# Optimization experiments

Hardware: AMD Instinct MI355X
Metric: run time of the kernel (lower is better)

The kernel has to match this reference:

```python
import jax, jax.numpy as jnp
import numpy as np
from jax import lax

INPUT_DIM = 16
H1 = 5
H2 = 50
NUM_CLASSES = 20
B = 4096
T = 512


def _lstm(x, w_ih, w_hh, b_ih, b_hh, hidden):
    # x: [B, T, D]; PyTorch LSTM gate order i, f, g, o; returns all hidden states [B, T, H]
    xg = jnp.einsum('btd,gd->btg', x, w_ih) + (b_ih + b_hh)  # [B, T, 4H]
    xg_t = jnp.swapaxes(xg, 0, 1)  # [T, B, 4H]
    h0 = jnp.zeros((x.shape[0], hidden), x.dtype)
    c0 = jnp.zeros((x.shape[0], hidden), x.dtype)

    def step(carry, xt):
        h, c = carry
        g = xt + h @ w_hh.T  # [B, 4H]
        i, f, gg, o = jnp.split(g, 4, axis=-1)
        i = jax.nn.sigmoid(i)
        f = jax.nn.sigmoid(f)
        gg = jnp.tanh(gg)
        o = jax.nn.sigmoid(o)
        c = f * c + i * gg
        h = o * jnp.tanh(c)
        return (h, c), h

    _, hs = lax.scan(step, (h0, c0), xg_t)
    return jnp.swapaxes(hs, 0, 1)  # [B, T, H]


def setup_inputs() -> dict:
    key = jax.random.key(0)
    ks = jax.random.split(key, 12)
    s1 = 1.0 / np.sqrt(H1)
    s2 = 1.0 / np.sqrt(H2)
    u = lambda k, shape, s: jax.random.uniform(k, shape, jnp.float32, -s, s)
    return {
        'x': jax.random.normal(ks[0], (B, T, INPUT_DIM), jnp.float32),
        'w_ih1': u(ks[1], (4 * H1, INPUT_DIM), s1),
        'w_hh1': u(ks[2], (4 * H1, H1), s1),
        'b_ih1': u(ks[3], (4 * H1,), s1),
        'b_hh1': u(ks[4], (4 * H1,), s1),
        'w_ih2': u(ks[5], (4 * H2, H1), s2),
        'w_hh2': u(ks[6], (4 * H2, H2), s2),
        'b_ih2': u(ks[7], (4 * H2,), s2),
        'b_hh2': u(ks[8], (4 * H2,), s2),
        'fc_w': u(ks[9], (NUM_CLASSES, H2), s2),
        'fc_b': u(ks[10], (NUM_CLASSES,), s2),
    }


def reference(x, w_ih1, w_hh1, b_ih1, b_hh1, w_ih2, w_hh2, b_ih2, b_hh2, fc_w, fc_b):
    h1 = _lstm(x, w_ih1, w_hh1, b_ih1, b_hh1, H1)   # [B, T, 5]
    h2 = _lstm(h1, w_ih2, w_hh2, b_ih2, b_hh2, H2)  # [B, T, 50]
    feat = h2[:, -1, :]  # last timestep; dropout is identity in eval mode
    out = feat @ fc_w.T + fc_b  # [B, num_classes]
    return (out, feat)
```

## Files before the change

### kernel.cpp

```cpp
#include <hip/hip_runtime.h>
#include <stdint.h>

#define B_TOTAL 4096
#define T_STEPS 512
#define IN_DIM 16
#define H1 5
#define H2 50
#define NCLS 20

typedef __attribute__((ext_vector_type(8))) short bf16x8;
typedef __attribute__((ext_vector_type(4))) float f32x4;

#define LOG2E 1.44269504f
#define C2L   2.88539008f

__device__ inline float rcp1pexp2(float y){
  return __builtin_amdgcn_rcpf(1.0f + __builtin_amdgcn_exp2f(y));
}

__device__ inline unsigned pack_top(float a, float b){
  return __builtin_amdgcn_perm(__float_as_uint(a), __float_as_uint(b), 0x07060302u);
}
__device__ inline void cvt_store(unsigned short* dh, unsigned short* dl, float4 v){
  uint2 H, L;
  H.x = pack_top(v.y, v.x);
  H.y = pack_top(v.w, v.z);
  float r0 = v.x - __uint_as_float(__float_as_uint(v.x) & 0xFFFF0000u);
  float r1 = v.y - __uint_as_float(__float_as_uint(v.y) & 0xFFFF0000u);
  float r2 = v.z - __uint_as_float(__float_as_uint(v.z) & 0xFFFF0000u);
  float r3 = v.w - __uint_as_float(__float_as_uint(v.w) & 0xFFFF0000u);
  L.x = pack_top(r1, r0);
  L.y = pack_top(r3, r2);
  *(uint2*)dh = H; *(uint2*)dl = L;
}
__device__ inline void split1(float h, unsigned short& hi, unsigned short& lo){
  unsigned u = __float_as_uint(h);
  hi = (unsigned short)(u >> 16);
  float r = h - __uint_as_float(u & 0xFFFF0000u);
  lo = (unsigned short)(__float_as_uint(r) >> 16);
}
__device__ inline void wsplit(float w, short& hi, short& lo){
  unsigned u = __float_as_uint(w);
  hi = (short)(u >> 16);
  float r = w - __uint_as_float(u & 0xFFFF0000u);
  lo = (short)(__float_as_uint(r) >> 16);
}

#define LDS_FENCE() __asm__ volatile("s_waitcnt lgkmcnt(0)" ::: "memory")
#define BARRIER()   __asm__ volatile("s_barrier" ::: "memory")

__global__ __launch_bounds__(320, 1) void lstm_fused_kernel(
    const float* __restrict__ x,
    const float* __restrict__ w_ih1, const float* __restrict__ w_hh1,
    const float* __restrict__ b_ih1, const float* __restrict__ b_hh1,
    const float* __restrict__ w_ih2, const float* __restrict__ w_hh2,
    const float* __restrict__ b_ih2, const float* __restrict__ b_hh2,
    const float* __restrict__ fc_w, const float* __restrict__ fc_b,
    float* __restrict__ out)
{
  const int tid  = threadIdx.x;
  const int lane = tid & 63;
  const int wave = tid >> 6;
  const int l15  = lane & 15;
  const int quad = lane >> 4;
  const int b0   = blockIdx.x * 16;

  __shared__ __align__(16) unsigned short a2h[2][16*72], a2l[2][16*72];
  __shared__ __align__(16) unsigned short xrh[8][16*24], xrl[8][16*24];
  __shared__ __align__(16) unsigned short a1h[16*24], a1l[16*24];
  __shared__ float h2f[16*52];

  bf16x8 Bh[4][2], Bl[4][2];
  float bias[4];
  float cst[4] = {0.f,0.f,0.f,0.f};
  const int cg = wave*16 + l15;

  if (wave < 4){
    bool valid = cg < H2;
#pragma unroll
    for (int tt=0; tt<4; ++tt){
      const float gsc = (tt == 2) ? C2L : LOG2E;
      int grow = tt*H2 + cg;
#pragma unroll
      for (int kt=0; kt<2; ++kt){
#pragma unroll
        for (int j=0;j<8;j++){
          int kk = kt*32 + quad*8 + j;
          float w = 0.f;
          if (valid){
            if (kk < H2)         w = w_hh2[grow*H2 + kk];
            else if (kk < H2+H1) w = w_ih2[grow*H1 + (kk-H2)];
          }
          w *= gsc;
          short hi, lo; wsplit(w, hi, lo);
          Bh[tt][kt][j] = hi; Bl[tt][kt][j] = lo;
        }
      }
      bias[tt] = valid ? gsc * (b_ih2[grow] + b_hh2[grow]) : 0.f;
    }
  } else {
    bool valid = l15 < H1;
#pragma unroll
    for (int tt=0; tt<4; ++tt){
      const float gsc = (tt == 2) ? C2L : LOG2E;
      int grow = tt*H1 + l15;
#pragma unroll
      for (int j=0;j<8;j++){
        int kk = quad*8 + j;
        float w = 0.f;
        if (valid){
          if (kk < IN_DIM)         w = w_ih1[grow*IN_DIM + kk];
          else if (kk < IN_DIM+H1) w = w_hh1[grow*H1 + (kk-IN_DIM)];
        }
        w *= gsc;
        short hi, lo; wsplit(w, hi, lo);
        Bh[tt][0][j] = hi; Bl[tt][0][j] = lo;
        Bh[tt][1][j] = 0;  Bl[tt][1][j] = 0;
      }
      bias[tt] = valid ? gsc * (b_ih1[grow] + b_hh1[grow]) : 0.f;
    }
  }

  f32x4 biasv[4];
#pragma unroll
  for (int tt=0; tt<4; ++tt){
    biasv[tt][0] = bias[tt]; biasv[tt][1] = bias[tt];
    biasv[tt][2] = bias[tt]; biasv[tt][3] = bias[tt];
  }
  const f32x4 zero4 = {0.f,0.f,0.f,0.f};

  { unsigned short* p = &a2h[0][0]; for (int i=tid;i<2*16*72;i+=320) p[i]=0; }
  { unsigned short* p = &a2l[0][0]; for (int i=tid;i<2*16*72;i+=320) p[i]=0; }
  { unsigned short* p = &a1h[0];    for (int i=tid;i<16*24;i+=320)   p[i]=0; }
  { unsigned short* p = &a1l[0];    for (int i=tid;i<16*24;i+=320)   p[i]=0; }

  const int xb = lane >> 2;
  const int xd = (lane & 3) * 4;
  if (wave == 4){
#pragma unroll
    for (int s=0;s<8;s++){
      float4 v = *(const float4*)&x[((size_t)(b0+xb)*T_STEPS + s)*IN_DIM + xd];
      cvt_store(&xrh[s][xb*24+xd], &xrl[s][xb*24+xd], v);
    }
  }
  __syncthreads();

  float4 pf0, pf1, pf2, pf3;
  bool pend = false;

#define ACT_BLOCK(ACC_, HV_) \
    _Pragma("unroll") \
    for (int r=0;r<4;r++){ \
      float gi = rcp1pexp2(-ACC_[0][r]); \
      float gf = rcp1pexp2(-ACC_[1][r]); \
      float gg = fmaf(-2.0f, rcp1pexp2(ACC_[2][r]), 1.0f); \
      float go = rcp1pexp2(-ACC_[3][r]); \
      cst[r] = fmaf(gf, cst[r], gi * (C2L * gg)); \
      HV_[r] = go * fmaf(-2.0f, rcp1pexp2(cst[r]), 1.0f); \
    }

#define LSTM2_BODY(T_, RD_, WR_) do { \
    const int rb = l15*72; \
    bf16x8 ah0 = *(const bf16x8*)&a2h[RD_][rb +      quad*8]; \
    bf16x8 al0 = *(const bf16x8*)&a2l[RD_][rb +      quad*8]; \
    bf16x8 ah1 = *(const bf16x8*)&a2h[RD_][rb + 32 + quad*8]; \
    bf16x8 al1 = *(const bf16x8*)&a2l[RD_][rb + 32 + quad*8]; \
    f32x4 acc[4]; \
    _Pragma("unroll") \
    for (int tt=0; tt<4; ++tt){ \
      f32x4 c0 = __builtin_amdgcn_mfma_f32_16x16x32_bf16(ah0, Bh[tt][0], biasv[tt], 0,0,0); \
      c0 = __builtin_amdgcn_mfma_f32_16x16x32_bf16(al0, Bh[tt][0], c0, 0,0,0); \
      c0 = __builtin_amdgcn_mfma_f32_16x16x32_bf16(ah0, Bl[tt][0], c0, 0,0,0); \
      f32x4 c1 = __builtin_amdgcn_mfma_f32_16x16x32_bf16(ah1, Bh[tt][1], zero4, 0,0,0); \
      c1 = __builtin_amdgcn_mfma_f32_16x16x32_bf16(al1, Bh[tt][1], c1, 0,0,0); \
      c1 = __builtin_amdgcn_mfma_f32_16x16x32_bf16(ah1, Bl[tt][1], c1, 0,0,0); \
      acc[tt] = c0 + c1; \
    } \
    float hv[4]; \
    ACT_BLOCK(acc, hv) \
    if (cg < H2){ \
      const int wrb = quad*4*72 + cg; \
      _Pragma("unroll") \
      for (int r=0;r<4;r++){ \
        unsigned short hh, hl; split1(hv[r], hh, hl); \
        a2h[WR_][wrb + r*72] = hh; \
        a2l[WR_][wrb + r*72] = hl; \
      } \
      if ((T_) == T_STEPS-1){ \
        _Pragma("unroll") \
        for (int r=0;r<4;r++){ \
          out[(size_t)B_TOTAL*NCLS + (size_t)(b0+quad*4+r)*H2 + cg] = hv[r]; \
          h2f[(quad*4+r)*52 + cg] = hv[r]; \
        } \
      } \
    } \
  } while(0)

#define LSTM1_BODY(T_, WR_) do { \
    const int s = (T_) + 1; \
    if (s < T_STEPS){ \
      if ((s & 3) == 0 && s+4 < T_STEPS){ \
        const float* xp = &x[((size_t)(b0+xb)*T_STEPS + (s+4))*IN_DIM + xd]; \
        pf0 = *(const float4*)(xp + 0*IN_DIM); \
        pf1 = *(const float4*)(xp + 1*IN_DIM); \
        pf2 = *(const float4*)(xp + 2*IN_DIM); \
        pf3 = *(const float4*)(xp + 3*IN_DIM); \
        pend = true; \
      } \
      const int slot = s & 7; \
      bf16x8 ah, al; \
      if (quad < 2){ \
        ah = *(const bf16x8*)&xrh[slot][l15*24 + quad*8]; \
        al = *(const bf16x8*)&xrl[slot][l15*24 + quad*8]; \
      } else { \
        ah = *(const bf16x8*)&a1h[l15*24 + (quad-2)*8]; \
        al = *(const bf16x8*)&a1l[l15*24 + (quad-2)*8]; \
      } \
      f32x4 acc[4]; \
      _Pragma("unroll") \
      for (int tt=0; tt<4; ++tt){ \
        f32x4 c0 = __builtin_amdgcn_mfma_f32_16x16x32_bf16(ah, Bh[tt][0], biasv[tt], 0,0,0); \
        c0 = __builtin_amdgcn_mfma_f32_16x16x32_bf16(al, Bh[tt][0], c0, 0,0,0); \
        c0 = __builtin_amdgcn_mfma_f32_16x16x32_bf16(ah, Bl[tt][0], c0, 0,0,0); \
        acc[tt] = c0; \
      } \
      float hv[4]; \
      ACT_BLOCK(acc, hv) \
      if (l15 < H1){ \
        _Pragma("unroll") \
        for (int r=0;r<4;r++){ \
          unsigned short hh, hl; split1(hv[r], hh, hl); \
          const int row = quad*4 + r; \
          a1h[row*24 + l15] = hh; \
          a1l[row*24 + l15] = hl; \
          a2h[WR_][row*72 + H2 + l15] = hh; \
          a2l[WR_][row*72 + H2 + l15] = hl; \
        } \
      } \
      if ((s & 3) == 2 && pend){ \
        cvt_store(&xrh[(s+2)&7][xb*24+xd], &xrl[(s+2)&7][xb*24+xd], pf0); \
        cvt_store(&xrh[(s+3)&7][xb*24+xd], &xrl[(s+3)&7][xb*24+xd], pf1); \
        cvt_store(&xrh[(s+4)&7][xb*24+xd], &xrl[(s+4)&7][xb*24+xd], pf2); \
        cvt_store(&xrh[(s+5)&7][xb*24+xd], &xrl[(s+5)&7][xb*24+xd], pf3); \
        pend = false; \
      } \
    } \
  } while(0)

  if (wave == 4) LSTM1_BODY(-1, 0);
  LDS_FENCE(); BARRIER();

  for (int t2 = 0; t2 < T_STEPS; t2 += 2){
    if (wave == 4) LSTM1_BODY(t2, 1);
    else           LSTM2_BODY(t2, 0, 1);
    LDS_FENCE(); BARRIER();
    if (wave == 4) LSTM1_BODY(t2+1, 0);
    else           LSTM2_BODY(t2+1, 1, 0);
    LDS_FENCE(); BARRIER();
  }

#undef LSTM2_BODY
#undef LSTM1_BODY
#undef ACT_BLOCK

  __syncthreads();
  {
    int b = tid / 20, o = tid % 20;
    float s = fc_b[o];
#pragma unroll 10
    for (int k=0;k<H2;k++) s += fc_w[o*H2+k] * h2f[b*52+k];
    out[(size_t)(b0+b)*NCLS + o] = s;
  }
}

extern "C" void kernel_launch(void* const* d_in, const int* in_sizes, int n_in,
                              void* d_out, int out_size, void* d_ws, size_t ws_size,
                              hipStream_t stream) {
  const float* x     = (const float*)d_in[0];
  const float* w_ih1 = (const float*)d_in[1];
  const float* w_hh1 = (const float*)d_in[2];
  const float* b_ih1 = (const float*)d_in[3];
  const float* b_hh1 = (const float*)d_in[4];
  const float* w_ih2 = (const float*)d_in[5];
  const float* w_hh2 = (const float*)d_in[6];
  const float* b_ih2 = (const float*)d_in[7];
  const float* b_hh2 = (const float*)d_in[8];
  const float* fc_w  = (const float*)d_in[9];
  const float* fc_b  = (const float*)d_in[10];
  float* out = (float*)d_out;

  lstm_fused_kernel<<<dim3(B_TOTAL/16), dim3(320), 0, stream>>>(
      x, w_ih1, w_hh1, b_ih1, b_hh1, w_ih2, w_hh2, b_ih2, b_hh2, fc_w, fc_b, out);
}
```

Baseline: 633.8 us.

## Fold layer-1 LSTM into fourth wave alongside last layer-2 columns, drop fifth wave

The block shrinks from five waves to four. Wave 3 now computes the last two layer-2 hidden columns and all five layer-1 units in the same MFMA tile, using a third K-slice for the x input. x is now kept in registers through a rotating two-step prefetch instead of being staged in LDS ring buffers. The tanh gate scale is folded into the fma constants. The intent is to cut the wave count per barrier and remove the LDS staging for x and h1. In exchange, wave 3 does 50% more MFMAs per step and may become the critical path.

Result: faster. 605.1 us (-4.5%).

```diff
diff --git a/kernel.cpp b/kernel.cpp
--- a/kernel.cpp
+++ b/kernel.cpp
@@ -13,26 +13,12 @@
 
 #define LOG2E 1.44269504f
 #define C2L   2.88539008f
+#define C2L2  5.77078016f
 
 __device__ inline float rcp1pexp2(float y){
   return __builtin_amdgcn_rcpf(1.0f + __builtin_amdgcn_exp2f(y));
 }
 
-__device__ inline unsigned pack_top(float a, float b){
-  return __builtin_amdgcn_perm(__float_as_uint(a), __float_as_uint(b), 0x07060302u);
-}
-__device__ inline void cvt_store(unsigned short* dh, unsigned short* dl, float4 v){
-  uint2 H, L;
-  H.x = pack_top(v.y, v.x);
-  H.y = pack_top(v.w, v.z);
-  float r0 = v.x - __uint_as_float(__float_as_uint(v.x) & 0xFFFF0000u);
-  float r1 = v.y - __uint_as_float(__float_as_uint(v.y) & 0xFFFF0000u);
-  float r2 = v.z - __uint_as_float(__float_as_uint(v.z) & 0xFFFF0000u);
-  float r3 = v.w - __uint_as_float(__float_as_uint(v.w) & 0xFFFF0000u);
-  L.x = pack_top(r1, r0);
-  L.y = pack_top(r3, r2);
-  *(uint2*)dh = H; *(uint2*)dl = L;
-}
 __device__ inline void split1(float h, unsigned short& hi, unsigned short& lo){
   unsigned u = __float_as_uint(h);
   hi = (unsigned short)(u >> 16);
@@ -45,11 +31,22 @@
   float r = w - __uint_as_float(u & 0xFFFF0000u);
   lo = (short)(__float_as_uint(r) >> 16);
 }
+__device__ inline void xsplit(float4 a, float4 b, bf16x8& H, bf16x8& L){
+  short h,l;
+  wsplit(a.x,h,l); H[0]=h; L[0]=l;
+  wsplit(a.y,h,l); H[1]=h; L[1]=l;
+  wsplit(a.z,h,l); H[2]=h; L[2]=l;
+  wsplit(a.w,h,l); H[3]=h; L[3]=l;
+  wsplit(b.x,h,l); H[4]=h; L[4]=l;
+  wsplit(b.y,h,l); H[5]=h; L[5]=l;
+  wsplit(b.z,h,l); H[6]=h; L[6]=l;
+  wsplit(b.w,h,l); H[7]=h; L[7]=l;
+}
 
 #define LDS_FENCE() __asm__ volatile("s_waitcnt lgkmcnt(0)" ::: "memory")
 #define BARRIER()   __asm__ volatile("s_barrier" ::: "memory")
 
-__global__ __launch_bounds__(320, 1) void lstm_fused_kernel(
+__global__ __launch_bounds__(256, 1) void lstm_fused_kernel(
     const float* __restrict__ x,
     const float* __restrict__ w_ih1, const float* __restrict__ w_hh1,
     const float* __restrict__ b_ih1, const float* __restrict__ b_hh1,
@@ -66,120 +63,157 @@
   const int b0   = blockIdx.x * 16;
 
   __shared__ __align__(16) unsigned short a2h[2][16*72], a2l[2][16*72];
-  __shared__ __align__(16) unsigned short xrh[8][16*24], xrl[8][16*24];
-  __shared__ __align__(16) unsigned short a1h[16*24], a1l[16*24];
   __shared__ float h2f[16*52];
 
-  bf16x8 Bh[4][2], Bl[4][2];
-  float bias[4];
+  const bf16x8 zero8 = {0,0,0,0,0,0,0,0};
+  const f32x4  zero4 = {0.f,0.f,0.f,0.f};
+
+  bf16x8 Bh[4][3], Bl[4][3];
+  f32x4 biasv[4];
   float cst[4] = {0.f,0.f,0.f,0.f};
-  const int cg = wave*16 + l15;
-
-  if (wave < 4){
-    bool valid = cg < H2;
+
+#pragma unroll
+  for (int tt=0; tt<4; ++tt)
+#pragma unroll
+    for (int kt=0; kt<3; ++kt){ Bh[tt][kt]=zero8; Bl[tt][kt]=zero8; }
+
+  if (wave < 3){
+    const int c = wave*16 + l15;
 #pragma unroll
     for (int tt=0; tt<4; ++tt){
       const float gsc = (tt == 2) ? C2L : LOG2E;
-      int grow = tt*H2 + cg;
+      const int grow = tt*H2 + c;
 #pragma unroll
       for (int kt=0; kt<2; ++kt){
 #pragma unroll
         for (int j=0;j<8;j++){
-          int kk = kt*32 + quad*8 + j;
+          const int kk = kt*32 + quad*8 + j;
           float w = 0.f;
-          if (valid){
-            if (kk < H2)         w = w_hh2[grow*H2 + kk];
-            else if (kk < H2+H1) w = w_ih2[grow*H1 + (kk-H2)];
-          }
+          if (kk < H2)         w = w_hh2[grow*H2 + kk];
+          else if (kk < H2+H1) w = w_ih2[grow*H1 + (kk-H2)];
           w *= gsc;
           short hi, lo; wsplit(w, hi, lo);
           Bh[tt][kt][j] = hi; Bl[tt][kt][j] = lo;
         }
       }
-      bias[tt] = valid ? gsc * (b_ih2[grow] + b_hh2[grow]) : 0.f;
+      const float bias = gsc * (b_ih2[grow] + b_hh2[grow]);
+      biasv[tt][0]=bias; biasv[tt][1]=bias; biasv[tt][2]=bias; biasv[tt][3]=bias;
     }
   } else {
-    bool valid = l15 < H1;
 #pragma unroll
     for (int tt=0; tt<4; ++tt){
       const float gsc = (tt == 2) ? C2L : LOG2E;
-      int grow = tt*H1 + l15;
-#pragma unroll
-      for (int j=0;j<8;j++){
-        int kk = quad*8 + j;
-        float w = 0.f;
-        if (valid){
-          if (kk < IN_DIM)         w = w_ih1[grow*IN_DIM + kk];
-          else if (kk < IN_DIM+H1) w = w_hh1[grow*H1 + (kk-IN_DIM)];
+      float bias = 0.f;
+      if (l15 < 2){
+        const int grow = tt*H2 + 48 + l15;
+#pragma unroll
+        for (int kt=0; kt<2; ++kt){
+#pragma unroll
+          for (int j=0;j<8;j++){
+            const int kk = kt*32 + quad*8 + j;
+            float w = 0.f;
+            if (kk < H2)         w = w_hh2[grow*H2 + kk];
+            else if (kk < H2+H1) w = w_ih2[grow*H1 + (kk-H2)];
+            w *= gsc;
+            short hi, lo; wsplit(w, hi, lo);
+            Bh[tt][kt][j] = hi; Bl[tt][kt][j] = lo;
+          }
         }
-        w *= gsc;
-        short hi, lo; wsplit(w, hi, lo);
-        Bh[tt][0][j] = hi; Bl[tt][0][j] = lo;
-        Bh[tt][1][j] = 0;  Bl[tt][1][j] = 0;
+        bias = gsc * (b_ih2[grow] + b_hh2[grow]);
+      } else if (l15 < 7){
+        const int e = l15 - 2;
+        const int grow = tt*H1 + e;
+#pragma unroll
+        for (int j=0;j<8;j++){
+          const int kk = 32 + quad*8 + j;
+          float w1 = (kk >= H2 && kk < H2+H1) ? gsc * w_hh1[grow*H1 + (kk-H2)] : 0.f;
+          short hi, lo; wsplit(w1, hi, lo);
+          Bh[tt][1][j] = hi; Bl[tt][1][j] = lo;
+          const int k2 = quad*8 + j;
+          float w2 = (k2 < IN_DIM) ? gsc * w_ih1[grow*IN_DIM + k2] : 0.f;
+          wsplit(w2, hi, lo);
+          Bh[tt][2][j] = hi; Bl[tt][2][j] = lo;
+        }
+        bias = gsc * (b_ih1[grow] + b_hh1[grow]);
       }
-      bias[tt] = valid ? gsc * (b_ih1[grow] + b_hh1[grow]) : 0.f;
-    }
-  }
-
-  f32x4 biasv[4];
-#pragma unroll
-  for (int tt=0; tt<4; ++tt){
-    biasv[tt][0] = bias[tt]; biasv[tt][1] = bias[tt];
-    biasv[tt][2] = bias[tt]; biasv[tt][3] = bias[tt];
-  }
-  const f32x4 zero4 = {0.f,0.f,0.f,0.f};
-
-  { unsigned short* p = &a2h[0][0]; for (int i=tid;i<2*16*72;i+=320) p[i]=0; }
-  { unsigned short* p = &a2l[0][0]; for (int i=tid;i<2*16*72;i+=320) p[i]=0; }
-  { unsigned short* p = &a1h[0];    for (int i=tid;i<16*24;i+=320)   p[i]=0; }
-  { unsigned short* p = &a1l[0];    for (int i=tid;i<16*24;i+=320)   p[i]=0; }
-
-  const int xb = lane >> 2;
-  const int xd = (lane & 3) * 4;
-  if (wave == 4){
-#pragma unroll
-    for (int s=0;s<8;s++){
-      float4 v = *(const float4*)&x[((size_t)(b0+xb)*T_STEPS + s)*IN_DIM + xd];
-      cvt_store(&xrh[s][xb*24+xd], &xrl[s][xb*24+xd], v);
-    }
+      biasv[tt][0]=bias; biasv[tt][1]=bias; biasv[tt][2]=bias; biasv[tt][3]=bias;
+    }
+  }
+
+  { unsigned short* p = &a2h[0][0]; for (int i=tid;i<2*16*72;i+=256) p[i]=0; }
+  { unsigned short* p = &a2l[0][0]; for (int i=tid;i<2*16*72;i+=256) p[i]=0; }
+
+  bf16x8 XAh = zero8, XAl = zero8, XBh = zero8, XBl = zero8;
+  float4 pa, pb;
+  const bool xact = (wave == 3) && (quad < 2);
+  const float* xbase = &x[(size_t)(b0+l15)*T_STEPS*IN_DIM + quad*8];
+  if (xact){
+    float4 a0 = *(const float4*)(xbase + 0);
+    float4 a1 = *(const float4*)(xbase + 4);
+    xsplit(a0, a1, XAh, XAl);
+    pa = *(const float4*)(xbase + 1*IN_DIM);
+    pb = *(const float4*)(xbase + 1*IN_DIM + 4);
   }
   __syncthreads();
 
-  float4 pf0, pf1, pf2, pf3;
-  bool pend = false;
+#define ROTATE(XH_, XL_, SN_) do { \
+    if (xact){ \
+      xsplit(pa, pb, XH_, XL_); \
+      const int sn_ = (SN_) < T_STEPS ? (SN_) : T_STEPS-1; \
+      const float* xp_ = xbase + (size_t)sn_*IN_DIM; \
+      pa = *(const float4*)xp_; \
+      pb = *(const float4*)(xp_ + 4); \
+    } } while(0)
 
 #define ACT_BLOCK(ACC_, HV_) \
     _Pragma("unroll") \
     for (int r=0;r<4;r++){ \
       float gi = rcp1pexp2(-ACC_[0][r]); \
       float gf = rcp1pexp2(-ACC_[1][r]); \
-      float gg = fmaf(-2.0f, rcp1pexp2(ACC_[2][r]), 1.0f); \
+      float gg = fmaf(-C2L2, rcp1pexp2(ACC_[2][r]), C2L);  \
       float go = rcp1pexp2(-ACC_[3][r]); \
-      cst[r] = fmaf(gf, cst[r], gi * (C2L * gg)); \
+      cst[r] = fmaf(gf, cst[r], gi * gg); \
       HV_[r] = go * fmaf(-2.0f, rcp1pexp2(cst[r]), 1.0f); \
     }
 
-#define LSTM2_BODY(T_, RD_, WR_) do { \
-    const int rb = l15*72; \
-    bf16x8 ah0 = *(const bf16x8*)&a2h[RD_][rb +      quad*8]; \
-    bf16x8 al0 = *(const bf16x8*)&a2l[RD_][rb +      quad*8]; \
-    bf16x8 ah1 = *(const bf16x8*)&a2h[RD_][rb + 32 + quad*8]; \
-    bf16x8 al1 = *(const bf16x8*)&a2l[RD_][rb + 32 + quad*8]; \
+#define MAIN_BODY(T_, RD_, WR_, XCH_, XCL_, XNH_, XNL_) do { \
+    const int rb_ = l15*72; \
+    bf16x8 ah0 = *(const bf16x8*)&a2h[RD_][rb_ +      quad*8]; \
+    bf16x8 al0 = *(const bf16x8*)&a2l[RD_][rb_ +      quad*8]; \
+    bf16x8 ah1 = *(const bf16x8*)&a2h[RD_][rb_ + 32 + quad*8]; \
+    bf16x8 al1 = *(const bf16x8*)&a2l[RD_][rb_ + 32 + quad*8]; \
+    if (wave == 3) ROTATE(XNH_, XNL_, (T_)+3);   \
     f32x4 acc[4]; \
-    _Pragma("unroll") \
-    for (int tt=0; tt<4; ++tt){ \
-      f32x4 c0 = __builtin_amdgcn_mfma_f32_16x16x32_bf16(ah0, Bh[tt][0], biasv[tt], 0,0,0); \
-      c0 = __builtin_amdgcn_mfma_f32_16x16x32_bf16(al0, Bh[tt][0], c0, 0,0,0); \
-      c0 = __builtin_amdgcn_mfma_f32_16x16x32_bf16(ah0, Bl[tt][0], c0, 0,0,0); \
-      f32x4 c1 = __builtin_amdgcn_mfma_f32_16x16x32_bf16(ah1, Bh[tt][1], zero4, 0,0,0); \
-      c1 = __builtin_amdgcn_mfma_f32_16x16x32_bf16(al1, Bh[tt][1], c1, 0,0,0); \
-      c1 = __builtin_amdgcn_mfma_f32_16x16x32_bf16(ah1, Bl[tt][1], c1, 0,0,0); \
-      acc[tt] = c0 + c1; \
+    if (wave < 3){ \
+      _Pragma("unroll") \
+      for (int tt=0; tt<4; ++tt){ \
+        f32x4 c0 = __builtin_amdgcn_mfma_f32_16x16x32_bf16(ah0, Bh[tt][0], biasv[tt], 0,0,0); \
+        c0 = __builtin_amdgcn_mfma_f32_16x16x32_bf16(al0, Bh[tt][0], c0, 0,0,0); \
+        c0 = __builtin_amdgcn_mfma_f32_16x16x32_bf16(ah0, Bl[tt][0], c0, 0,0,0); \
+        f32x4 c1 = __builtin_amdgcn_mfma_f32_16x16x32_bf16(ah1, Bh[tt][1], zero4, 0,0,0); \
+        c1 = __builtin_amdgcn_mfma_f32_16x16x32_bf16(al1, Bh[tt][1], c1, 0,0,0); \
+        c1 = __builtin_amdgcn_mfma_f32_16x16x32_bf16(ah1, Bl[tt][1], c1, 0,0,0); \
+        acc[tt] = c0 + c1; \
+      } \
+    } else { \
+      _Pragma("unroll") \
+      for (int tt=0; tt<4; ++tt){ \
+        f32x4 c0 = __builtin_amdgcn_mfma_f32_16x16x32_bf16(ah0, Bh[tt][0], biasv[tt], 0,0,0); \
+        c0 = __builtin_amdgcn_mfma_f32_16x16x32_bf16(al0, Bh[tt][0], c0, 0,0,0); \
+        c0 = __builtin_amdgcn_mfma_f32_16x16x32_bf16(ah0, Bl[tt][0], c0, 0,0,0); \
+        f32x4 c1 = __builtin_amdgcn_mfma_f32_16x16x32_bf16(ah1, Bh[tt][1], zero4, 0,0,0); \
+        c1 = __builtin_amdgcn_mfma_f32_16x16x32_bf16(al1, Bh[tt][1], c1, 0,0,0); \
+        c1 = __builtin_amdgcn_mfma_f32_16x16x32_bf16(ah1, Bl[tt][1], c1, 0,0,0); \
+        f32x4 c2 = __builtin_amdgcn_mfma_f32_16x16x32_bf16(XCH_, Bh[tt][2], zero4, 0,0,0); \
+        c2 = __builtin_amdgcn_mfma_f32_16x16x32_bf16(XCL_, Bh[tt][2], c2, 0,0,0); \
+        c2 = __builtin_amdgcn_mfma_f32_16x16x32_bf16(XCH_, Bl[tt][2], c2, 0,0,0); \
+        acc[tt] = (c0 + c1) + c2; \
+      } \
     } \
     float hv[4]; \
     ACT_BLOCK(acc, hv) \
-    if (cg < H2){ \
-      const int wrb = quad*4*72 + cg; \
+    if (wave < 3){ \
+      const int wrb = quad*4*72 + wave*16 + l15; \
       _Pragma("unroll") \
       for (int r=0;r<4;r++){ \
         unsigned short hh, hl; split1(hv[r], hh, hl); \
@@ -189,83 +223,72 @@
       if ((T_) == T_STEPS-1){ \
         _Pragma("unroll") \
         for (int r=0;r<4;r++){ \
-          out[(size_t)B_TOTAL*NCLS + (size_t)(b0+quad*4+r)*H2 + cg] = hv[r]; \
-          h2f[(quad*4+r)*52 + cg] = hv[r]; \
+          out[(size_t)B_TOTAL*NCLS + (size_t)(b0+quad*4+r)*H2 + wave*16+l15] = hv[r]; \
+          h2f[(quad*4+r)*52 + wave*16+l15] = hv[r]; \
+        } \
+      } \
+    } else if (l15 < 7){ \
+      const int wrb = quad*4*72 + 48 + l15;   \
+      _Pragma("unroll") \
+      for (int r=0;r<4;r++){ \
+        unsigned short hh, hl; split1(hv[r], hh, hl); \
+        a2h[WR_][wrb + r*72] = hh; \
+        a2l[WR_][wrb + r*72] = hl; \
+      } \
+      if ((T_) == T_STEPS-1 && l15 < 2){ \
+        _Pragma("unroll") \
+        for (int r=0;r<4;r++){ \
+          out[(size_t)B_TOTAL*NCLS + (size_t)(b0+quad*4+r)*H2 + 48+l15] = hv[r]; \
+          h2f[(quad*4+r)*52 + 48+l15] = hv[r]; \
         } \
       } \
     } \
   } while(0)
 
-#define LSTM1_BODY(T_, WR_) do { \
-    const int s = (T_) + 1; \
-    if (s < T_STEPS){ \
-      if ((s & 3) == 0 && s+4 < T_STEPS){ \
-        const float* xp = &x[((size_t)(b0+xb)*T_STEPS + (s+4))*IN_DIM + xd]; \
-        pf0 = *(const float4*)(xp + 0*IN_DIM); \
-        pf1 = *(const float4*)(xp + 1*IN_DIM); \
-        pf2 = *(const float4*)(xp + 2*IN_DIM); \
-        pf3 = *(const float4*)(xp + 3*IN_DIM); \
-        pend = true; \
-      } \
-      const int slot = s & 7; \
-      bf16x8 ah, al; \
-      if (quad < 2){ \
-        ah = *(const bf16x8*)&xrh[slot][l15*24 + quad*8]; \
-        al = *(const bf16x8*)&xrl[slot][l15*24 + quad*8]; \
-      } else { \
-        ah = *(const bf16x8*)&a1h[l15*24 + (quad-2)*8]; \
-        al = *(const bf16x8*)&a1l[l15*24 + (quad-2)*8]; \
-      } \
-      f32x4 acc[4]; \
-      _Pragma("unroll") \
-      for (int tt=0; tt<4; ++tt){ \
-        f32x4 c0 = __builtin_amdgcn_mfma_f32_16x16x32_bf16(ah, Bh[tt][0], biasv[tt], 0,0,0); \
-        c0 = __builtin_amdgcn_mfma_f32_16x16x32_bf16(al, Bh[tt][0], c0, 0,0,0); \
-        c0 = __builtin_amdgcn_mfma_f32_16x16x32_bf16(ah, Bl[tt][0], c0, 0,0,0); \
-        acc[tt] = c0; \
-      } \
-      float hv[4]; \
-      ACT_BLOCK(acc, hv) \
-      if (l15 < H1){ \
-        _Pragma("unroll") \
-        for (int r=0;r<4;r++){ \
-          unsigned short hh, hl; split1(hv[r], hh, hl); \
-          const int row = quad*4 + r; \
-          a1h[row*24 + l15] = hh; \
-          a1l[row*24 + l15] = hl; \
-          a2h[WR_][row*72 + H2 + l15] = hh; \
-          a2l[WR_][row*72 + H2 + l15] = hl; \
-        } \
-      } \
-      if ((s & 3) == 2 && pend){ \
-        cvt_store(&xrh[(s+2)&7][xb*24+xd], &xrl[(s+2)&7][xb*24+xd], pf0); \
-        cvt_store(&xrh[(s+3)&7][xb*24+xd], &xrl[(s+3)&7][xb*24+xd], pf1); \
-        cvt_store(&xrh[(s+4)&7][xb*24+xd], &xrl[(s+4)&7][xb*24+xd], pf2); \
-        cvt_store(&xrh[(s+5)&7][xb*24+xd], &xrl[(s+5)&7][xb*24+xd], pf3); \
-        pend = false; \
-      } \
-    } \
-  } while(0)
-
-  if (wave == 4) LSTM1_BODY(-1, 0);
+  if (wave == 3){
+    f32x4 acc[4];
+#pragma unroll
+    for (int tt=0; tt<4; ++tt){
+      f32x4 c2 = __builtin_amdgcn_mfma_f32_16x16x32_bf16(XAh, Bh[tt][2], biasv[tt], 0,0,0);
+      c2 = __builtin_amdgcn_mfma_f32_16x16x32_bf16(XAl, Bh[tt][2], c2, 0,0,0);
+      c2 = __builtin_amdgcn_mfma_f32_16x16x32_bf16(XAh, Bl[tt][2], c2, 0,0,0);
+      acc[tt] = c2;
+    }
+    ROTATE(XBh, XBl, 2);
+    const bool isl1 = (l15 >= 2) && (l15 < 7);
+#pragma unroll
+    for (int r=0;r<4;r++){
+      float gi = rcp1pexp2(-acc[0][r]);
+      float gf = rcp1pexp2(-acc[1][r]);
+      float gg = fmaf(-C2L2, rcp1pexp2(acc[2][r]), C2L);
+      float go = rcp1pexp2(-acc[3][r]);
+      float cn = fmaf(gf, cst[r], gi * gg);
+      if (isl1){
+        cst[r] = cn;
+        float h = go * fmaf(-2.0f, rcp1pexp2(cn), 1.0f);
+        unsigned short hh, hl; split1(h, hh, hl);
+        const int row = quad*4 + r;
+        a2h[0][row*72 + 48 + l15] = hh;
+        a2l[0][row*72 + 48 + l15] = hl;
+      }
+    }
+  }
   LDS_FENCE(); BARRIER();
 
   for (int t2 = 0; t2 < T_STEPS; t2 += 2){
-    if (wave == 4) LSTM1_BODY(t2, 1);
-    else           LSTM2_BODY(t2, 0, 1);
+    MAIN_BODY(t2,   0, 1, XBh, XBl, XAh, XAl);
     LDS_FENCE(); BARRIER();
-    if (wave == 4) LSTM1_BODY(t2+1, 0);
-    else           LSTM2_BODY(t2+1, 1, 0);
+    MAIN_BODY(t2+1, 1, 0, XAh, XAl, XBh, XBl);
     LDS_FENCE(); BARRIER();
   }
 
-#undef LSTM2_BODY
-#undef LSTM1_BODY
+#undef MAIN_BODY
 #undef ACT_BLOCK
+#undef ROTATE
 
   __syncthreads();
-  {
-    int b = tid / 20, o = tid % 20;
+  for (int i = tid; i < 16*NCLS; i += 256){
+    const int b = i / NCLS, o = i % NCLS;
     float s = fc_b[o];
 #pragma unroll 10
     for (int k=0;k<H2;k++) s += fc_w[o*H2+k] * h2f[b*52+k];
@@ -289,6 +312,6 @@
   const float* fc_b  = (const float*)d_in[10];
   float* out = (float*)d_out;
 
-  lstm_fused_kernel<<<dim3(B_TOTAL/16), dim3(320), 0, stream>>>(
+  lstm_fused_kernel<<<dim3(B_TOTAL/16), dim3(256), 0, stream>>>(
       x, w_ih1, w_hh1, b_ih1, b_hh1, w_ih2, w_hh2, b_ih2, b_hh2, fc_w, fc_b, out);
 }
```
